# Kernel optimization log

Hardware: AMD Instinct MI355X
Metric: run time of the kernel (lower is better)

The kernel has to match this reference:

```python
import jax, jax.numpy as jnp
import numpy as np

B, T, D = 4, 2048, 1024
H, HS = 16, 64  # num heads, head size; H*HS == D


def setup_inputs() -> dict:
    key = jax.random.key(0)
    ks = jax.random.split(key, 6)
    scale = D ** -0.5
    x = jax.random.normal(ks[0], (B, T, D), dtype=jnp.float32)
    # per-head projections, stacked: [H, D, HS]
    Wq = jax.random.normal(ks[1], (H, D, HS), dtype=jnp.float32) * scale
    Wk = jax.random.normal(ks[2], (H, D, HS), dtype=jnp.float32) * scale
    Wv = jax.random.normal(ks[3], (H, D, HS), dtype=jnp.float32) * scale
    # output projection: [H*HS, D] + bias [D]
    Wp = jax.random.normal(ks[4], (H * HS, D), dtype=jnp.float32) * ((H * HS) ** -0.5)
    bp = jax.random.normal(ks[5], (D,), dtype=jnp.float32) * 0.01
    return {"x": x, "Wq": Wq, "Wk": Wk, "Wv": Wv, "Wp": Wp, "bp": bp}


def reference(x, Wq, Wk, Wv, Wp, bp):
    # per-head Q, K, V projections (batched over heads): [B, H, T, HS]
    q = jnp.einsum('btd,hde->bhte', x, Wq)
    k = jnp.einsum('btd,hde->bhte', x, Wk)
    v = jnp.einsum('btd,hde->bhte', x, Wv)
    # scaled scores with causal mask: [B, H, T, T]
    scores = jnp.einsum('bhte,bhse->bhts', q, k) * (HS ** -0.5)
    causal = jnp.tril(jnp.ones((T, T), dtype=bool))
    scores = jnp.where(causal, scores, jnp.float32(-jnp.inf))
    wei = jax.nn.softmax(scores, axis=-1)  # dropout is identity at eval
    out = jnp.einsum('bhts,bhse->bhte', wei, v)
    # concat heads -> [B, T, H*HS], then output projection
    out = out.transpose(0, 2, 1, 3).reshape(B, T, H * HS)
    return out @ Wp + bp
```

## Files before the change

kernel.cpp:

```cpp
#include <hip/hip_runtime.h>
#include <stdint.h>

typedef __attribute__((ext_vector_type(8))) short short8;
typedef __attribute__((ext_vector_type(4))) float f32x4;
typedef __attribute__((ext_vector_type(16))) float f32x16;

__device__ __forceinline__ unsigned short f2bf(float f) {
  unsigned u = __float_as_uint(f);
  u = u + 0x7FFFu + ((u >> 16) & 1u);
  return (unsigned short)(u >> 16);
}
__device__ __forceinline__ unsigned cvtpk_bf16(float lo, float hi) {
  unsigned r;
  asm("v_cvt_pk_bf16_f32 %0, %1, %2" : "=v"(r) : "v"(lo), "v"(hi));
  return r;
}
__device__ __forceinline__ float fast_exp2(float x) {
#if __has_builtin(__builtin_amdgcn_exp2f)
  return __builtin_amdgcn_exp2f(x);
#else
  return exp2f(x);
#endif
}
__device__ __forceinline__ void gl2lds16(const void* g, void* l) {
  __builtin_amdgcn_global_load_lds(
      (const __attribute__((address_space(1))) void*)(uintptr_t)g,
      (__attribute__((address_space(3))) void*)(uintptr_t)l, 16, 0, 0);
}

__global__ __launch_bounds__(256) void pack_all_kernel(const float* __restrict__ x,
                                                       const float* __restrict__ Wq,
                                                       const float* __restrict__ Wk,
                                                       const float* __restrict__ Wv,
                                                       const float* __restrict__ Wp,
                                                       ushort* __restrict__ xb,
                                                       ushort* __restrict__ WqkvT,
                                                       ushort* __restrict__ WpT) {
  __shared__ float tile[64][65];
  const int bid0 = blockIdx.x;
  const int tid = threadIdx.x;
  if (bid0 < 4096) {
    int i = (bid0 * 256 + tid) * 8;
    float4 a = *(const float4*)(x + i);
    float4 b = *(const float4*)(x + i + 4);
    uint4 o;
    o.x = (unsigned)f2bf(a.x) | ((unsigned)f2bf(a.y) << 16);
    o.y = (unsigned)f2bf(a.z) | ((unsigned)f2bf(a.w) << 16);
    o.z = (unsigned)f2bf(b.x) | ((unsigned)f2bf(b.y) << 16);
    o.w = (unsigned)f2bf(b.z) | ((unsigned)f2bf(b.w) << 16);
    *(uint4*)(xb + i) = o;
    return;
  }
  const int bid = bid0 - 4096;
  const int lr = tid >> 6;
  const int lc = tid & 63;
  if (bid < 768) {
    const int s = bid >> 8;
    const int rem = bid & 255;
    const int h = rem >> 4;
    const int dt = rem & 15;
    const float* W = (s == 0) ? Wq : (s == 1) ? Wk : Wv;
    const float scale = (s == 0) ? 0.18033688011f : 1.0f;
#pragma unroll
    for (int p = 0; p < 16; ++p) {
      int r = p * 4 + lr;
      tile[r][lc] = W[(size_t)(h * 1024 + dt * 64 + r) * 64 + lc];
    }
    __syncthreads();
#pragma unroll
    for (int p = 0; p < 16; ++p) {
      int e = p * 4 + lr;
      float v = tile[lc][e] * scale;
      WqkvT[(size_t)(s * 1024 + h * 64 + e) * 1024 + dt * 64 + lc] = f2bf(v);
    }
  } else {
    const int t = bid - 768;
    const int rt = t >> 4, ct = t & 15;
#pragma unroll
    for (int p = 0; p < 16; ++p) {
      int r = p * 4 + lr;
      tile[r][lc] = Wp[(size_t)(rt * 64 + r) * 1024 + ct * 64 + lc];
    }
    __syncthreads();
#pragma unroll
    for (int p = 0; p < 16; ++p) {
      int c = p * 4 + lr;
      float v = tile[lc][c];
      WpT[(size_t)(ct * 64 + c) * 1024 + rt * 64 + lc] = f2bf(v);
    }
  }
}

template <int OUT_MODE>
__global__ __launch_bounds__(256) void gemm_bt(const ushort* __restrict__ A,
                                               const ushort* __restrict__ BT,
                                               ushort* __restrict__ Cb,
                                               float* __restrict__ Cf,
                                               const float* __restrict__ bias,
                                               int M, int N, int K) {
  __shared__ __align__(16) ushort Al[3][128 * 32];
  __shared__ __align__(16) ushort Bl[3][128 * 32];
  const int tid = threadIdx.x;
  const int lane = tid & 63;
  const int wave = tid >> 6;
  const int wm = wave >> 1, wn = wave & 1;
  const int nbx = gridDim.x;
  const int nwg = nbx * gridDim.y;
  int wg = blockIdx.y * nbx + blockIdx.x;
  wg = (wg & 7) * (nwg >> 3) + (wg >> 3);
  const int m0 = (wg / nbx) * 128, n0 = (wg % nbx) * 128;
  const int r16 = lane & 15, g = lane >> 4;
  f32x4 acc[4][4] = {};
  const int kTiles = K >> 5;
  const size_t ldb = (size_t)K * 2;
  const int srow = tid >> 2;
  const int scolsw = ((tid & 3) * 16) ^ ((srow & 3) << 4);
  const char* a_src = (const char*)A + (size_t)(m0 + srow) * ldb + scolsw;
  const char* b_src = (const char*)BT + (size_t)(n0 + srow) * ldb + scolsw;
  const size_t half = (size_t)64 * ldb;
  char* a_d0 = (char*)&Al[0][0] + wave * 1024;
  char* b_d0 = (char*)&Bl[0][0] + wave * 1024;

#define STAGE(kt, slot)                                        \
  {                                                            \
    const int k0b = (kt) * 64;                                 \
    gl2lds16(a_src + k0b, a_d0 + (slot)*8192);                 \
    gl2lds16(a_src + half + k0b, a_d0 + (slot)*8192 + 4096);   \
    gl2lds16(b_src + k0b, b_d0 + (slot)*8192);                 \
    gl2lds16(b_src + half + k0b, b_d0 + (slot)*8192 + 4096);   \
  }

  STAGE(0, 0);
  STAGE(1, 1);
  asm volatile("s_waitcnt vmcnt(4)" ::: "memory");
  __builtin_amdgcn_s_barrier();

  int slot = 0;
  const int swf = (r16 & 3) << 4;
  for (int kt = 0; kt < kTiles; ++kt) {
    const int nslot = (slot == 0) ? 2 : slot - 1;
    if (kt + 2 < kTiles) STAGE(kt + 2, nslot);
    const char* Ab = (const char*)&Al[slot][0];
    const char* Bb = (const char*)&Bl[slot][0];
    short8 af[4], bfr[4];
#pragma unroll
    for (int i = 0; i < 4; ++i) {
      af[i] = *(const short8*)(Ab + (wm * 64 + i * 16 + r16) * 64 + ((g * 16) ^ swf));
      bfr[i] = *(const short8*)(Bb + (wn * 64 + i * 16 + r16) * 64 + ((g * 16) ^ swf));
    }
#pragma unroll
    for (int mi = 0; mi < 4; ++mi)
#pragma unroll
      for (int ni = 0; ni < 4; ++ni)
        acc[mi][ni] =
            __builtin_amdgcn_mfma_f32_16x16x32_bf16(af[mi], bfr[ni], acc[mi][ni], 0, 0, 0);
    if (kt + 2 < kTiles) {
      asm volatile("s_waitcnt vmcnt(4)" ::: "memory");
    } else {
      asm volatile("s_waitcnt vmcnt(0)" ::: "memory");
    }
    __builtin_amdgcn_s_barrier();
    slot = (slot == 2) ? 0 : slot + 1;
  }
#undef STAGE

#pragma unroll
  for (int mi = 0; mi < 4; ++mi)
#pragma unroll
    for (int ni = 0; ni < 4; ++ni)
#pragma unroll
      for (int r = 0; r < 4; ++r) {
        int row = m0 + wm * 64 + mi * 16 + g * 4 + r;
        int col = n0 + wn * 64 + ni * 16 + r16;
        float v = acc[mi][ni][r];
        if (OUT_MODE == 0) {
          Cb[(size_t)row * N + col] = f2bf(v);
        } else {
          Cf[(size_t)row * N + col] = v + bias[col];
        }
      }
}

__global__ __launch_bounds__(256) void attn_mfma_kernel(const ushort* __restrict__ QKV,
                                                        ushort* __restrict__ O) {
  int flat = blockIdx.z * 128 + blockIdx.y * 8 + blockIdx.x;
  flat = (flat & 7) * 64 + (flat >> 3);
  const int qtA = flat & 7;
  const int h = (flat >> 3) & 15;
  const int b = flat >> 7;
  __shared__ __align__(16) ushort Kl[64 * 64];
  __shared__ __align__(16) ushort VT[64 * 64];
  const int tid = threadIdx.x;
  const int lane = tid & 63;
  const int wave = tid >> 6;
  const int lo5 = lane & 31;
  const int hi = lane >> 5;

  short8 ones;
#pragma unroll
  for (int i = 0; i < 8; ++i) ones[i] = (short)0x3F80;

  const int k_key0 = wave * 16 + (lane >> 3);
  const int k_key1 = k_key0 + 8;
  const int ksrc_off0 = ((lane & 7) * 16) ^ ((k_key0 & 7) << 4);
  const int ksrc_off1 = ((lane & 7) * 16) ^ ((k_key1 & 7) << 4);
  const char* kgbase = (const char*)(QKV + ((size_t)b * 2048) * 3072 + 1024 + h * 64);
  const int kp2 = (tid & 31) * 2;
  const int dg = tid >> 5;
  const char* vgbase = (const char*)(QKV + ((size_t)b * 2048) * 3072 + 2048 + h * 64 + dg * 8);

#pragma unroll
  for (int ph = 0; ph < 2; ++ph) {
    const int qt = ph ? qtA : (15 - qtA);
    const int qbase = qt * 128 + wave * 32;
    const int qg = qbase + lo5;

    short8 qf[4];
    {
      const ushort* qp = QKV + ((size_t)(b * 2048 + qbase + lo5) * 3072) + h * 64 + hi * 8;
#pragma unroll
      for (int dc = 0; dc < 4; ++dc) qf[dc] = *(const short8*)(qp + dc * 16);
    }

    f32x16 o0 = {}, o1 = {}, lacc = {};
    const int nblk = qt * 2 + 2;

    uint4 nv0, nv1;
    {
      const char* vp = vgbase + (size_t)kp2 * 6144;
      nv0 = *(const uint4*)(vp);
      nv1 = *(const uint4*)(vp + 6144);
    }

    for (int blk = 0; blk < nblk; ++blk) {
      const int s0 = blk * 64;
      __syncthreads();
      {
        const ushort* e0 = (const ushort*)&nv0;
        const ushort* e1 = (const ushort*)&nv1;
#pragma unroll
        for (int j = 0; j < 8; ++j) {
          const int row = dg * 8 + j;
          *(unsigned*)((char*)VT + row * 128 + ((kp2 * 2) ^ ((row & 7) << 4))) =
              (unsigned)e0[j] | ((unsigned)e1[j] << 16);
        }
      }
      gl2lds16(kgbase + (size_t)(s0 + k_key0) * 6144 + ksrc_off0, (char*)Kl + wave * 2048);
      gl2lds16(kgbase + (size_t)(s0 + k_key1) * 6144 + ksrc_off1,
               (char*)Kl + wave * 2048 + 1024);
      __syncthreads();

      if (blk + 1 < nblk) {
        const char* vp = vgbase + (size_t)(s0 + 64 + kp2) * 6144;
        nv0 = *(const uint4*)(vp);
        nv1 = *(const uint4*)(vp + 6144);
      }

#pragma unroll
      for (int g2 = 0; g2 < 2; ++g2) {
        const int ks = s0 + g2 * 32;
        if (ks > qbase + 31) continue;
        f32x16 s_acc = {};
        const int krow = g2 * 32 + lo5;
        const char* ksrc = (const char*)Kl + krow * 128;
        const int ksw = (krow & 7) << 4;
#pragma unroll
        for (int dc = 0; dc < 4; ++dc) {
          short8 kf = *(const short8*)(ksrc + ((dc * 32 + hi * 16) ^ ksw));
          s_acc = __builtin_amdgcn_mfma_f32_32x32x16_bf16(kf, qf[dc], s_acc, 0, 0, 0);
        }
        float p[16];
        if (ks + 31 > qbase) {
          const int ksg = ks + 4 * hi;
#pragma unroll
          for (int r = 0; r < 16; ++r) {
            const int key_g = ksg + (r & 3) + 8 * (r >> 2);
            float pv = fast_exp2(s_acc[r]);
            p[r] = (key_g <= qg) ? pv : 0.f;
          }
        } else {
#pragma unroll
          for (int r = 0; r < 16; ++r) p[r] = fast_exp2(s_acc[r]);
        }
#pragma unroll
        for (int kc = 0; kc < 2; ++kc) {
          unsigned w0 = cvtpk_bf16(p[kc * 8 + 0], p[kc * 8 + 1]);
          unsigned w2 = cvtpk_bf16(p[kc * 8 + 4], p[kc * 8 + 5]);
          unsigned w1 = cvtpk_bf16(p[kc * 8 + 2], p[kc * 8 + 3]);
          unsigned w3 = cvtpk_bf16(p[kc * 8 + 6], p[kc * 8 + 7]);
          asm("v_permlane32_swap_b32 %0, %1" : "+v"(w0), "+v"(w2));
          asm("v_permlane32_swap_b32 %0, %1" : "+v"(w1), "+v"(w3));
          uint4 paw;
          paw.x = w0; paw.y = w1; paw.z = w2; paw.w = w3;
          short8 pa = *(short8*)&paw;
          const int kb = (g2 * 32 + kc * 16 + hi * 8) * 2;
          lacc = __builtin_amdgcn_mfma_f32_32x32x16_bf16(pa, ones, lacc, 0, 0, 0);
          {
            const int vrow = lo5;
            short8 vf =
                *(const short8*)((const char*)VT + vrow * 128 + (kb ^ ((vrow & 7) << 4)));
            o0 = __builtin_amdgcn_mfma_f32_32x32x16_bf16(pa, vf, o0, 0, 0, 0);
          }
          {
            const int vrow = 32 + lo5;
            short8 vf =
                *(const short8*)((const char*)VT + vrow * 128 + (kb ^ ((vrow & 7) << 4)));
            o1 = __builtin_amdgcn_mfma_f32_32x32x16_bf16(pa, vf, o1, 0, 0, 0);
          }
        }
      }
    }

#pragma unroll
    for (int r = 0; r < 16; ++r) {
      const int qr = (r & 3) + 8 * (r >> 2) + 4 * hi;
      const float li = 1.f / lacc[r];
      ushort* ob = O + ((size_t)(b * 2048 + qbase + qr) * 1024) + h * 64 + lo5;
      ob[0] = f2bf(o0[r] * li);
      ob[32] = f2bf(o1[r] * li);
    }
  }
}

extern "C" void kernel_launch(void* const* d_in, const int* in_sizes, int n_in,
                              void* d_out, int out_size, void* d_ws, size_t ws_size,
                              hipStream_t stream) {
  const float* x = (const float*)d_in[0];
  const float* Wq = (const float*)d_in[1];
  const float* Wk = (const float*)d_in[2];
  const float* Wv = (const float*)d_in[3];
  const float* Wp = (const float*)d_in[4];
  const float* bp = (const float*)d_in[5];
  float* out = (float*)d_out;

  ushort* xb = (ushort*)d_ws;
  ushort* WqkvT = xb + 8388608;
  ushort* WpT = WqkvT + 3145728;
  ushort* QKV = WpT + 1048576;
  ushort* O = QKV + 25165824;

  pack_all_kernel<<<5120, 256, 0, stream>>>(x, Wq, Wk, Wv, Wp, xb, WqkvT, WpT);
  gemm_bt<0><<<dim3(24, 64), 256, 0, stream>>>(xb, WqkvT, QKV, nullptr, nullptr,
                                               8192, 3072, 1024);
  attn_mfma_kernel<<<dim3(8, 16, 4), 256, 0, stream>>>(QKV, O);
  gemm_bt<1><<<dim3(8, 64), 256, 0, stream>>>(O, WpT, nullptr, out, bp,
                                              8192, 1024, 1024);
}
```

Measured before the change: 166.9 us.

## Use single-buffered BK=64 GEMM tiles and 2-wave attention blocks with 64-row Q tiles

The GEMM drops its 3-slot async pipeline for a single LDS buffer holding 64-wide K tiles, synchronizing twice per tile and issuing two MFMA k-steps per tile. The attention kernel moves from 4-wave blocks covering 128 query rows to 2-wave blocks covering 64 rows. That doubles the grid and adjusts the K/V LDS fill loops for the smaller thread count. The GEMM change cuts barrier count but gives up overlap of global loads with compute. The attention change aims at finer load balance and higher occupancy, at the cost of less K/V reuse per block.

Result: no change. 164.8 us (-1.3%).

```diff
diff --git a/kernel.cpp b/kernel.cpp
--- a/kernel.cpp
+++ b/kernel.cpp
@@ -98,8 +98,8 @@
                                                float* __restrict__ Cf,
                                                const float* __restrict__ bias,
                                                int M, int N, int K) {
-  __shared__ __align__(16) ushort Al[3][128 * 32];
-  __shared__ __align__(16) ushort Bl[3][128 * 32];
+  __shared__ __align__(16) ushort Al[128 * 64];
+  __shared__ __align__(16) ushort Bl[128 * 64];
   const int tid = threadIdx.x;
   const int lane = tid & 63;
   const int wave = tid >> 6;
@@ -111,59 +111,45 @@
   const int m0 = (wg / nbx) * 128, n0 = (wg % nbx) * 128;
   const int r16 = lane & 15, g = lane >> 4;
   f32x4 acc[4][4] = {};
-  const int kTiles = K >> 5;
+  const int kTiles = K >> 6;
   const size_t ldb = (size_t)K * 2;
-  const int srow = tid >> 2;
-  const int scolsw = ((tid & 3) * 16) ^ ((srow & 3) << 4);
-  const char* a_src = (const char*)A + (size_t)(m0 + srow) * ldb + scolsw;
-  const char* b_src = (const char*)BT + (size_t)(n0 + srow) * ldb + scolsw;
-  const size_t half = (size_t)64 * ldb;
-  char* a_d0 = (char*)&Al[0][0] + wave * 1024;
-  char* b_d0 = (char*)&Bl[0][0] + wave * 1024;
-
-#define STAGE(kt, slot)                                        \
-  {                                                            \
-    const int k0b = (kt) * 64;                                 \
-    gl2lds16(a_src + k0b, a_d0 + (slot)*8192);                 \
-    gl2lds16(a_src + half + k0b, a_d0 + (slot)*8192 + 4096);   \
-    gl2lds16(b_src + k0b, b_d0 + (slot)*8192);                 \
-    gl2lds16(b_src + half + k0b, b_d0 + (slot)*8192 + 4096);   \
+  const int srow = tid >> 3;
+  const int scol = ((tid & 7) * 16) ^ (((tid >> 3) & 7) << 4);
+  const char* a_src = (const char*)A + (size_t)(m0 + srow) * ldb + scol;
+  const char* b_src = (const char*)BT + (size_t)(n0 + srow) * ldb + scol;
+  char* a_d = (char*)Al + wave * 1024;
+  char* b_d = (char*)Bl + wave * 1024;
+  const size_t row32 = (size_t)32 * ldb;
+  for (int kt = 0; kt < kTiles; ++kt) {
+    const size_t k0b = (size_t)kt * 128;
+    if (kt) __syncthreads();
+#pragma unroll
+    for (int i = 0; i < 4; ++i) {
+      gl2lds16(a_src + i * row32 + k0b, a_d + i * 4096);
+      gl2lds16(b_src + i * row32 + k0b, b_d + i * 4096);
+    }
+    __syncthreads();
+    short8 af[4][2], bf2[4][2];
+#pragma unroll
+    for (int i = 0; i < 4; ++i) {
+      const int ra = (wm * 64 + i * 16 + r16) * 128;
+      const int rb = (wn * 64 + i * 16 + r16) * 128;
+      const int sw = (r16 & 7) << 4;
+#pragma unroll
+      for (int ks = 0; ks < 2; ++ks) {
+        af[i][ks] = *(const short8*)((const char*)Al + ra + ((ks * 64 + g * 16) ^ sw));
+        bf2[i][ks] = *(const short8*)((const char*)Bl + rb + ((ks * 64 + g * 16) ^ sw));
+      }
+    }
+#pragma unroll
+    for (int ks = 0; ks < 2; ++ks)
+#pragma unroll
+      for (int mi = 0; mi < 4; ++mi)
+#pragma unroll
+        for (int ni = 0; ni < 4; ++ni)
+          acc[mi][ni] = __builtin_amdgcn_mfma_f32_16x16x32_bf16(af[mi][ks], bf2[ni][ks],
+                                                                acc[mi][ni], 0, 0, 0);
   }
-
-  STAGE(0, 0);
-  STAGE(1, 1);
-  asm volatile("s_waitcnt vmcnt(4)" ::: "memory");
-  __builtin_amdgcn_s_barrier();
-
-  int slot = 0;
-  const int swf = (r16 & 3) << 4;
-  for (int kt = 0; kt < kTiles; ++kt) {
-    const int nslot = (slot == 0) ? 2 : slot - 1;
-    if (kt + 2 < kTiles) STAGE(kt + 2, nslot);
-    const char* Ab = (const char*)&Al[slot][0];
-    const char* Bb = (const char*)&Bl[slot][0];
-    short8 af[4], bfr[4];
-#pragma unroll
-    for (int i = 0; i < 4; ++i) {
-      af[i] = *(const short8*)(Ab + (wm * 64 + i * 16 + r16) * 64 + ((g * 16) ^ swf));
-      bfr[i] = *(const short8*)(Bb + (wn * 64 + i * 16 + r16) * 64 + ((g * 16) ^ swf));
-    }
-#pragma unroll
-    for (int mi = 0; mi < 4; ++mi)
-#pragma unroll
-      for (int ni = 0; ni < 4; ++ni)
-        acc[mi][ni] =
-            __builtin_amdgcn_mfma_f32_16x16x32_bf16(af[mi], bfr[ni], acc[mi][ni], 0, 0, 0);
-    if (kt + 2 < kTiles) {
-      asm volatile("s_waitcnt vmcnt(4)" ::: "memory");
-    } else {
-      asm volatile("s_waitcnt vmcnt(0)" ::: "memory");
-    }
-    __builtin_amdgcn_s_barrier();
-    slot = (slot == 2) ? 0 : slot + 1;
-  }
-#undef STAGE
-
 #pragma unroll
   for (int mi = 0; mi < 4; ++mi)
 #pragma unroll
@@ -181,13 +167,13 @@
       }
 }
 
-__global__ __launch_bounds__(256) void attn_mfma_kernel(const ushort* __restrict__ QKV,
+__global__ __launch_bounds__(128) void attn_mfma_kernel(const ushort* __restrict__ QKV,
                                                         ushort* __restrict__ O) {
-  int flat = blockIdx.z * 128 + blockIdx.y * 8 + blockIdx.x;
-  flat = (flat & 7) * 64 + (flat >> 3);
-  const int qtA = flat & 7;
-  const int h = (flat >> 3) & 15;
-  const int b = flat >> 7;
+  int flat = blockIdx.z * 256 + blockIdx.y * 16 + blockIdx.x;
+  flat = (flat & 7) * 128 + (flat >> 3);
+  const int qtA = flat & 15;
+  const int h = (flat >> 4) & 15;
+  const int b = flat >> 8;
   __shared__ __align__(16) ushort Kl[64 * 64];
   __shared__ __align__(16) ushort VT[64 * 64];
   const int tid = threadIdx.x;
@@ -200,19 +186,17 @@
 #pragma unroll
   for (int i = 0; i < 8; ++i) ones[i] = (short)0x3F80;
 
-  const int k_key0 = wave * 16 + (lane >> 3);
-  const int k_key1 = k_key0 + 8;
-  const int ksrc_off0 = ((lane & 7) * 16) ^ ((k_key0 & 7) << 4);
-  const int ksrc_off1 = ((lane & 7) * 16) ^ ((k_key1 & 7) << 4);
+  const int krow_off = wave * 8 + (lane >> 3);
+  const int ksrc_col = ((lane & 7) * 16) ^ (((lane >> 3) & 7) << 4);
   const char* kgbase = (const char*)(QKV + ((size_t)b * 2048) * 3072 + 1024 + h * 64);
   const int kp2 = (tid & 31) * 2;
-  const int dg = tid >> 5;
-  const char* vgbase = (const char*)(QKV + ((size_t)b * 2048) * 3072 + 2048 + h * 64 + dg * 8);
+  const int dg0 = tid >> 5;
+  const char* vgbase = (const char*)(QKV + ((size_t)b * 2048) * 3072 + 2048 + h * 64);
 
 #pragma unroll
   for (int ph = 0; ph < 2; ++ph) {
-    const int qt = ph ? qtA : (15 - qtA);
-    const int qbase = qt * 128 + wave * 32;
+    const int qt = ph ? qtA : (31 - qtA);
+    const int qbase = qt * 64 + wave * 32;
     const int qg = qbase + lo5;
 
     short8 qf[4];
@@ -223,37 +207,47 @@
     }
 
     f32x16 o0 = {}, o1 = {}, lacc = {};
-    const int nblk = qt * 2 + 2;
-
-    uint4 nv0, nv1;
+    const int nblk = qt + 1;
+
+    uint4 va0, va1, vb0, vb1;
     {
-      const char* vp = vgbase + (size_t)kp2 * 6144;
-      nv0 = *(const uint4*)(vp);
-      nv1 = *(const uint4*)(vp + 6144);
+      const char* vp = vgbase + (size_t)kp2 * 6144 + dg0 * 16;
+      va0 = *(const uint4*)vp;
+      va1 = *(const uint4*)(vp + 6144);
+      vb0 = *(const uint4*)(vp + 64);
+      vb1 = *(const uint4*)(vp + 6144 + 64);
     }
 
     for (int blk = 0; blk < nblk; ++blk) {
       const int s0 = blk * 64;
       __syncthreads();
       {
-        const ushort* e0 = (const ushort*)&nv0;
-        const ushort* e1 = (const ushort*)&nv1;
+        const ushort* ea0 = (const ushort*)&va0;
+        const ushort* ea1 = (const ushort*)&va1;
+        const ushort* eb0 = (const ushort*)&vb0;
+        const ushort* eb1 = (const ushort*)&vb1;
 #pragma unroll
         for (int j = 0; j < 8; ++j) {
-          const int row = dg * 8 + j;
-          *(unsigned*)((char*)VT + row * 128 + ((kp2 * 2) ^ ((row & 7) << 4))) =
-              (unsigned)e0[j] | ((unsigned)e1[j] << 16);
-        }
-      }
-      gl2lds16(kgbase + (size_t)(s0 + k_key0) * 6144 + ksrc_off0, (char*)Kl + wave * 2048);
-      gl2lds16(kgbase + (size_t)(s0 + k_key1) * 6144 + ksrc_off1,
-               (char*)Kl + wave * 2048 + 1024);
+          const int col = (kp2 * 2) ^ (j << 4);
+          *(unsigned*)((char*)VT + (dg0 * 8 + j) * 128 + col) =
+              (unsigned)ea0[j] | ((unsigned)ea1[j] << 16);
+          *(unsigned*)((char*)VT + ((dg0 + 4) * 8 + j) * 128 + col) =
+              (unsigned)eb0[j] | ((unsigned)eb1[j] << 16);
+        }
+      }
+#pragma unroll
+      for (int i = 0; i < 4; ++i) {
+        gl2lds16(kgbase + (size_t)(s0 + i * 16 + krow_off) * 6144 + ksrc_col,
+                 (char*)Kl + i * 2048 + wave * 1024);
+      }
       __syncthreads();
 
       if (blk + 1 < nblk) {
-        const char* vp = vgbase + (size_t)(s0 + 64 + kp2) * 6144;
-        nv0 = *(const uint4*)(vp);
-        nv1 = *(const uint4*)(vp + 6144);
+        const char* vp = vgbase + (size_t)(s0 + 64 + kp2) * 6144 + dg0 * 16;
+        va0 = *(const uint4*)vp;
+        va1 = *(const uint4*)(vp + 6144);
+        vb0 = *(const uint4*)(vp + 64);
+        vb1 = *(const uint4*)(vp + 6144 + 64);
       }
 
 #pragma unroll
@@ -342,7 +336,7 @@
   pack_all_kernel<<<5120, 256, 0, stream>>>(x, Wq, Wk, Wv, Wp, xb, WqkvT, WpT);
   gemm_bt<0><<<dim3(24, 64), 256, 0, stream>>>(xb, WqkvT, QKV, nullptr, nullptr,
                                                8192, 3072, 1024);
-  attn_mfma_kernel<<<dim3(8, 16, 4), 256, 0, stream>>>(QKV, O);
+  attn_mfma_kernel<<<dim3(16, 16, 4), 128, 0, stream>>>(QKV, O);
   gemm_bt<1><<<dim3(8, 64), 256, 0, stream>>>(O, WpT, nullptr, out, bp,
                                               8192, 1024, 1024);
 }
```
